# Kernel tuning notes

Hardware: AMD Instinct MI355X
Metric: run time of the kernel (lower is better)

## Reference

```python
import jax, jax.numpy as jnp
import numpy as np

DIM = 512
NH, NKV, HD = 8, 4, DIM // 8
KVD = NKV * HD
EPS = 1.1920928955078125e-07  # torch.finfo(float32).eps (F.rms_norm default)
ROPE_BASE = 10000.0


def _rms_norm(x):
    # F.rms_norm over last dim, no learned weight
    ms = jnp.mean(jnp.square(x), axis=-1, keepdims=True)
    return x * jax.lax.rsqrt(ms + EPS)


def _rope_tables(T, dtype):
    inv_freq = 1.0 / (ROPE_BASE ** (jnp.arange(0, HD, 2, dtype=jnp.float32) / HD))
    t = jnp.arange(T, dtype=jnp.float32)
    f = jnp.outer(t, inv_freq)  # [T, HD//2]
    return jnp.cos(f).astype(dtype)[None, None], jnp.sin(f).astype(dtype)[None, None]


def _apply_rot(x, c, s):
    h = x.shape[-1] // 2
    x1, x2 = x[..., :h], x[..., h:]
    return jnp.concatenate((x1 * c + x2 * s, -x1 * s + x2 * c), axis=-1)


def setup_inputs() -> dict:
    key = jax.random.key(0)
    ks = jax.random.split(key, 5)
    B, T = 8, 2048
    x = jax.random.normal(ks[0], (B, T, DIM), dtype=jnp.float32)
    # torch Linear weights: [out_features, in_features]
    Wq = jax.random.normal(ks[1], (DIM, DIM), dtype=jnp.float32) * (DIM ** -0.5)
    Wk = jax.random.normal(ks[2], (KVD, DIM), dtype=jnp.float32) * (DIM ** -0.5)
    Wv = jax.random.normal(ks[3], (KVD, DIM), dtype=jnp.float32) * (DIM ** -0.5)
    Wp = jax.random.normal(ks[4], (DIM, DIM), dtype=jnp.float32) * (DIM ** -0.5)
    return {"x": x, "Wq": Wq, "Wk": Wk, "Wv": Wv, "Wp": Wp}


def reference(x, Wq, Wk, Wv, Wp):
    B, T, C = x.shape
    q = (x @ Wq.T).reshape(B, T, NH, HD).transpose(0, 2, 1, 3)    # [B,NH,T,HD]
    k = (x @ Wk.T).reshape(B, T, NKV, HD).transpose(0, 2, 1, 3)   # [B,NKV,T,HD]
    v = (x @ Wv.T).reshape(B, T, NKV, HD).transpose(0, 2, 1, 3)
    q, k = _rms_norm(q), _rms_norm(k)
    c, s = _rope_tables(T, q.dtype)
    q, k = _apply_rot(q, c, s), _apply_rot(k, c, s)
    rep = NH // NKV
    k = jnp.repeat(k, rep, axis=1)  # GQA expand -> [B,NH,T,HD]
    v = jnp.repeat(v, rep, axis=1)
    scale = 1.0 / jnp.sqrt(jnp.asarray(HD, dtype=q.dtype))
    scores = jnp.einsum('bhqd,bhkd->bhqk', q, k) * scale
    causal = jnp.tril(jnp.ones((T, T), dtype=bool))
    scores = jnp.where(causal[None, None], scores, jnp.finfo(scores.dtype).min)
    attn = jax.nn.softmax(scores, axis=-1)
    y = jnp.einsum('bhqk,bhkd->bhqd', attn, v)
    y = y.transpose(0, 2, 1, 3).reshape(B, T, C)
    return y @ Wp.T
```

## Files before the change

### kernel.cpp

```cpp
#include <hip/hip_runtime.h>
#include <hip/hip_bf16.h>
#include <stdint.h>

typedef __bf16 bf16;
typedef __bf16 bf16x8 __attribute__((ext_vector_type(8)));
typedef __bf16 bf16x4 __attribute__((ext_vector_type(4)));
typedef float f32x4 __attribute__((ext_vector_type(4)));

#define T_SEQ 2048
#define DIM_ 512
#define NH_ 8
#define NKV_ 4
#define HD_ 64
#define BT_ (8 * T_SEQ)
#define NEG_INF (-1e30f)
#define EPS_ 1.1920928955078125e-07f
#define QSCALE 0.18033688011112042f
#define SMAX 12.0f

#define OFF_XB   (size_t)(0)
#define OFF_WQKV (size_t)(16777216)
#define OFF_WP   (size_t)(17825792)
#define OFF_COS  (size_t)(18350080)
#define OFF_SIN  (size_t)(18612224)
#define OFF_QT   (size_t)(18874368)
#define OFF_KT   (size_t)(35651584)
#define OFF_VT   (size_t)(44040192)
#define OFF_Y    (size_t)(52428800)
#define WS_NEEDED (size_t)(69206016)

__device__ inline void mfma16(f32x4& acc, bf16x8 a, bf16x8 b) {
    acc = __builtin_amdgcn_mfma_f32_16x16x32_bf16(a, b, acc, 0, 0, 0);
}

typedef const __attribute__((address_space(1))) uint8_t* gas_ptr;
typedef __attribute__((address_space(3))) uint8_t* las_ptr;
__device__ inline void gload16(const bf16* g, bf16* l) {
    __builtin_amdgcn_global_load_lds((gas_ptr)(const void*)g, (las_ptr)(void*)l, 16, 0, 0);
}

__global__ void prep_kernel(const float* __restrict__ x, const float* __restrict__ wq,
                            const float* __restrict__ wk, const float* __restrict__ wv,
                            const float* __restrict__ wp,
                            bf16* __restrict__ xb, bf16* __restrict__ wqkv,
                            bf16* __restrict__ wpb, float* __restrict__ cosT,
                            float* __restrict__ sinT) {
    int tid = blockIdx.x * blockDim.x + threadIdx.x;
    int stride = gridDim.x * blockDim.x;
    for (int i = tid; i < BT_ * DIM_; i += stride) xb[i] = (bf16)x[i];
    for (int i = tid; i < 1024 * 512; i += stride) {
        int j = i >> 9, k = i & 511;
        float v;
        if (j < 512) v = wq[i];
        else if (j < 768) v = wk[(j - 512) * 512 + k];
        else v = wv[(j - 768) * 512 + k];
        wqkv[i] = (bf16)v;
    }
    for (int i = tid; i < 512 * 512; i += stride) wpb[i] = (bf16)wp[i];
    for (int i = tid; i < T_SEQ * 32; i += stride) {
        int t = i >> 5, d = i & 31;
        float inv = powf(10000.0f, -(float)d * (1.0f / 32.0f));
        float f = (float)t * inv;
        cosT[i] = cosf(f);
        sinT[i] = sinf(f);
    }
}

__global__ __launch_bounds__(256) void qkv_gemm(const bf16* __restrict__ A,
                                                const bf16* __restrict__ B,
                                                bf16* __restrict__ qt,
                                                bf16* __restrict__ kt,
                                                bf16* __restrict__ vt,
                                                const float* __restrict__ cosT,
                                                const float* __restrict__ sinT) {
    __shared__ __align__(16) char smem[34816];
    bf16* As = (bf16*)smem;
    bf16* Bs = (bf16*)(smem + 16384);
    const int tid = threadIdx.x, lane = tid & 63, wid = tid >> 6;
    const int wr = wid >> 1, wc = wid & 1;
    const int lm = lane & 15, hi = lane >> 4;
    const int bid = blockIdx.x;
    const int swz = (bid & 7) * 128 + (bid >> 3);
    const int brow = (swz & 127) * 128;
    const int bcol = (swz >> 7) * 128;

    f32x4 acc[4][4] = {};
    for (int k0 = 0; k0 < 512; k0 += 64) {
        __syncthreads();
#pragma unroll
        for (int i = 0; i < 4; ++i) {
            int c = i * 256 + tid;
            int slot = c >> 6, l = c & 63;
            int row = (slot >> 1) * 16 + (l & 15);
            int kc = (slot & 1) * 32 + (l >> 4) * 8;
            gload16(A + (size_t)(brow + row) * 512 + k0 + kc, As + c * 8);
            gload16(B + (size_t)(bcol + row) * 512 + k0 + kc, Bs + c * 8);
        }
        asm volatile("s_waitcnt vmcnt(0)" ::: "memory");
        __syncthreads();
#pragma unroll
        for (int kk = 0; kk < 2; ++kk) {
            bf16x8 af[4], bfr[4];
#pragma unroll
            for (int m = 0; m < 4; ++m)
                af[m] = *(const bf16x8*)(As + (((wr * 4 + m) * 2 + kk) * 64 + lane) * 8);
#pragma unroll
            for (int n = 0; n < 4; ++n)
                bfr[n] = *(const bf16x8*)(Bs + (((wc * 4 + n) * 2 + kk) * 64 + lane) * 8);
            __builtin_amdgcn_s_setprio(1);
#pragma unroll
            for (int m = 0; m < 4; ++m)
#pragma unroll
                for (int n = 0; n < 4; ++n) mfma16(acc[m][n], af[m], bfr[n]);
            __builtin_amdgcn_s_setprio(0);
        }
    }
    __syncthreads();

    bf16* Tb = (bf16*)smem + wid * 4224;
    const int wcol = bcol + wc * 64;
    const int ctype = (wcol < 512) ? 0 : (wcol < 768 ? 1 : 2);

    if (ctype < 2) {
#pragma unroll
        for (int m = 0; m < 4; ++m)
#pragma unroll
            for (int r = 0; r < 4; ++r) {
                float v0 = acc[m][0][r], v1 = acc[m][1][r];
                float v2 = acc[m][2][r], v3 = acc[m][3][r];
                float ss = v0 * v0 + v1 * v1 + v2 * v2 + v3 * v3;
                ss += __shfl_xor(ss, 1);
                ss += __shfl_xor(ss, 2);
                ss += __shfl_xor(ss, 4);
                ss += __shfl_xor(ss, 8);
                float rinv = rsqrtf(ss * (1.0f / 64.0f) + EPS_);
                v0 *= rinv; v1 *= rinv; v2 *= rinv; v3 *= rinv;
                int rl = m * 16 + hi * 4 + r;
                int t = (brow + wr * 64 + rl) & (T_SEQ - 1);
                float c0 = cosT[t * 32 + lm], s0 = sinT[t * 32 + lm];
                float c1 = cosT[t * 32 + 16 + lm], s1 = sinT[t * 32 + 16 + lm];
                float o0 = v0 * c0 + v2 * s0;
                float o2 = v2 * c0 - v0 * s0;
                float o1 = v1 * c1 + v3 * s1;
                float o3 = v3 * c1 - v1 * s1;
                if (ctype == 0) { o0 *= QSCALE; o1 *= QSCALE; o2 *= QSCALE; o3 *= QSCALE; }
                Tb[rl * 66 + lm]      = (bf16)o0;
                Tb[rl * 66 + 16 + lm] = (bf16)o1;
                Tb[rl * 66 + 32 + lm] = (bf16)o2;
                Tb[rl * 66 + 48 + lm] = (bf16)o3;
            }
    } else {
#pragma unroll
        for (int m = 0; m < 4; ++m)
#pragma unroll
            for (int n = 0; n < 4; ++n)
#pragma unroll
                for (int r = 0; r < 4; ++r)
                    Tb[(n * 16 + lm) * 66 + m * 16 + hi * 4 + r] = (bf16)acc[m][n][r];
    }
    __syncthreads();

    const int i0 = brow + wr * 64;
    const int b = i0 >> 11, tt = i0 & (T_SEQ - 1);
#pragma unroll
    for (int p = 0; p < 8; ++p) {
        int row = p * 8 + (lane >> 3);
        int ch = lane & 7;
        bf16x8 val = *(const bf16x8*)(Tb + row * 66 + ch * 8);
        if (ctype == 0) {
            int head = wcol >> 6;
            *(bf16x8*)(qt + ((size_t)((b << 3) + head) * T_SEQ + tt + row) * 64 + ch * 8) = val;
        } else if (ctype == 1) {
            int head = (wcol - 512) >> 6;
            *(bf16x8*)(kt + ((size_t)((b << 2) + head) * T_SEQ + tt + row) * 64 + ch * 8) = val;
        } else {
            int head = (wcol - 768) >> 6;
            *(bf16x8*)(vt + ((size_t)((b << 2) + head) * 64 + row) * T_SEQ + tt + ch * 8) = val;
        }
    }
}

__global__ __launch_bounds__(256, 4) void attn_kernel(const bf16* __restrict__ qt,
                                                      const bf16* __restrict__ kt,
                                                      const bf16* __restrict__ vt,
                                                      bf16* __restrict__ y) {
    __shared__ bf16 Klds[4096];
    __shared__ bf16 Vlds[4096];
    __shared__ bf16 Plds[4][32 * 40];
    const int tid = threadIdx.x;
    const int lane = tid & 63, wid = tid >> 6;
    const int lm = lane & 15, hi = lane >> 4;
    const int bh = blockIdx.x & 63;
    const int p = 15 - (int)(blockIdx.x >> 6);
    const int b = bh >> 3, h = bh & 7, hv = h >> 1;
    const bf16* Q = qt + (size_t)bh * T_SEQ * HD_;
    const bf16* K = kt + (size_t)(b * NKV_ + hv) * T_SEQ * HD_;
    const bf16* V = vt + (size_t)(b * NKV_ + hv) * HD_ * T_SEQ;
    const int qB = p * 128;
    const int qw = qB + wid * 32;
    bf16* Pl = &Plds[wid][0];

    const int sl0 = tid >> 6, l0 = tid & 63;
    const int gr0 = (sl0 >> 1) * 16 + (l0 & 15);
    const int gc0 = (sl0 & 1) * 32 + (l0 >> 4) * 8;
    const int sl1 = (256 + tid) >> 6;
    const int gr1 = (sl1 >> 1) * 16 + (l0 & 15);
    const int gc1 = (sl1 & 1) * 32 + (l0 >> 4) * 8;
    const bf16* kg0 = K + (size_t)gr0 * HD_ + gc0;
    const bf16* kg1 = K + (size_t)gr1 * HD_ + gc1;
    const bf16* vg0 = V + (size_t)gr0 * T_SEQ + gc0;
    const bf16* vg1 = V + (size_t)gr1 * T_SEQ + gc1;
    bf16* kd0 = Klds + (size_t)tid * 8;
    bf16* kd1 = Klds + (size_t)(256 + tid) * 8;
    bf16* vd0 = Vlds + (size_t)tid * 8;
    bf16* vd1 = Vlds + (size_t)(256 + tid) * 8;

    bf16x8 qf[2][2];
#pragma unroll
    for (int qm = 0; qm < 2; ++qm)
#pragma unroll
        for (int kk = 0; kk < 2; ++kk)
            qf[qm][kk] = *(const bf16x8*)(Q + (size_t)(qw + 16 * qm + lm) * HD_ + 32 * kk + 8 * hi);

    f32x4 o[2][4] = {};
    float lrow[2] = {0.f, 0.f};

    const int nt = (qB >> 6) + 2;
    for (int t = 0; t < nt; ++t) {
        const int kv0 = t << 6;
        __syncthreads();
        {
            size_t ko = (size_t)kv0 * HD_, vo = (size_t)kv0;
            gload16(kg0 + ko, kd0);
            gload16(kg1 + ko, kd1);
            gload16(vg0 + vo, vd0);
            gload16(vg1 + vo, vd1);
        }
        asm volatile("s_waitcnt vmcnt(0)" ::: "memory");
        __syncthreads();

        if (kv0 <= qw + 31) {
            f32x4 s[2][4] = {};
#pragma unroll
            for (int kk = 0; kk < 2; ++kk) {
                bf16x8 kf[4];
#pragma unroll
                for (int n = 0; n < 4; ++n)
                    kf[n] = *(const bf16x8*)(Klds + ((n * 2 + kk) * 64 + lane) * 8);
#pragma unroll
                for (int qm = 0; qm < 2; ++qm)
#pragma unroll
                    for (int n = 0; n < 4; ++n) mfma16(s[qm][n], kf[n], qf[qm][kk]);
            }
            const bool partial = (kv0 + 63 > qw);
            bf16x4 pw[2][4];
#pragma unroll
            for (int qm = 0; qm < 2; ++qm) {
                const int qg = qw + 16 * qm + lm;
                float ps = 0.f;
#pragma unroll
                for (int n = 0; n < 4; ++n)
#pragma unroll
                    for (int r = 0; r < 4; ++r) {
                        float xv = s[qm][n][r];
                        if (partial)
                            xv = ((kv0 + 16 * n + 4 * hi + r) <= qg) ? xv : NEG_INF;
                        float e = __builtin_amdgcn_exp2f(xv - SMAX);
                        ps += e;
                        pw[qm][n][r] = (bf16)e;
                    }
                ps += __shfl_xor(ps, 16);
                ps += __shfl_xor(ps, 32);
                lrow[qm] += ps;
            }
#pragma unroll
            for (int kk = 0; kk < 2; ++kk) {
#pragma unroll
                for (int qm = 0; qm < 2; ++qm) {
                    *(bf16x4*)(Pl + (16 * qm + lm) * 40 + 4 * hi)      = pw[qm][2 * kk];
                    *(bf16x4*)(Pl + (16 * qm + lm) * 40 + 16 + 4 * hi) = pw[qm][2 * kk + 1];
                }
                bf16x8 vf[4], pf[2];
#pragma unroll
                for (int qm = 0; qm < 2; ++qm)
                    pf[qm] = *(const bf16x8*)(Pl + (16 * qm + lm) * 40 + 8 * hi);
#pragma unroll
                for (int nd = 0; nd < 4; ++nd)
                    vf[nd] = *(const bf16x8*)(Vlds + ((nd * 2 + kk) * 64 + lane) * 8);
#pragma unroll
                for (int qm = 0; qm < 2; ++qm)
#pragma unroll
                    for (int nd = 0; nd < 4; ++nd) mfma16(o[qm][nd], vf[nd], pf[qm]);
            }
        }
    }

#pragma unroll
    for (int qm = 0; qm < 2; ++qm) {
        float rcl = 1.0f / lrow[qm];
#pragma unroll
        for (int nd = 0; nd < 4; ++nd) {
            bf16x4 ov;
#pragma unroll
            for (int r = 0; r < 4; ++r) ov[r] = (bf16)(o[qm][nd][r] * rcl);
            *(bf16x4*)(Pl + lm * 72 + nd * 16 + 4 * hi) = ov;
        }
#pragma unroll
        for (int it = 0; it < 2; ++it) {
            int chunk = it * 64 + lane;
            int row = chunk >> 3, dc = (chunk & 7) * 8;
            bf16x8 val = *(const bf16x8*)(Pl + row * 72 + dc);
            *(bf16x8*)(y + (size_t)(b * T_SEQ + qw + 16 * qm + row) * DIM_ + h * HD_ + dc) = val;
        }
    }
}

__global__ __launch_bounds__(256) void proj_gemm(const bf16* __restrict__ A,
                                                 const bf16* __restrict__ B,
                                                 float* __restrict__ out) {
    __shared__ __align__(16) char smem[32768];
    bf16* As = (bf16*)smem;
    bf16* Bs = (bf16*)(smem + 16384);
    const int tid = threadIdx.x, lane = tid & 63, wid = tid >> 6;
    const int wr = wid >> 1, wc = wid & 1;
    const int lm = lane & 15, hi = lane >> 4;
    const int bid = blockIdx.x;
    const int swz = (bid & 7) * 64 + (bid >> 3);
    const int brow = (swz & 127) * 128;
    const int bcol = (swz >> 7) * 128;

    f32x4 acc[4][4] = {};
    for (int k0 = 0; k0 < 512; k0 += 64) {
        __syncthreads();
#pragma unroll
        for (int i = 0; i < 4; ++i) {
            int c = i * 256 + tid;
            int slot = c >> 6, l = c & 63;
            int row = (slot >> 1) * 16 + (l & 15);
            int kc = (slot & 1) * 32 + (l >> 4) * 8;
            gload16(A + (size_t)(brow + row) * 512 + k0 + kc, As + c * 8);
            gload16(B + (size_t)(bcol + row) * 512 + k0 + kc, Bs + c * 8);
        }
        asm volatile("s_waitcnt vmcnt(0)" ::: "memory");
        __syncthreads();
#pragma unroll
        for (int kk = 0; kk < 2; ++kk) {
            bf16x8 af[4], bfr[4];
#pragma unroll
            for (int m = 0; m < 4; ++m)
                af[m] = *(const bf16x8*)(As + (((wr * 4 + m) * 2 + kk) * 64 + lane) * 8);
#pragma unroll
            for (int n = 0; n < 4; ++n)
                bfr[n] = *(const bf16x8*)(Bs + (((wc * 4 + n) * 2 + kk) * 64 + lane) * 8);
            __builtin_amdgcn_s_setprio(1);
#pragma unroll
            for (int m = 0; m < 4; ++m)
#pragma unroll
                for (int n = 0; n < 4; ++n) mfma16(acc[m][n], af[m], bfr[n]);
            __builtin_amdgcn_s_setprio(0);
        }
    }
#pragma unroll
    for (int m = 0; m < 4; ++m)
#pragma unroll
        for (int n = 0; n < 4; ++n)
#pragma unroll
            for (int r = 0; r < 4; ++r) {
                int i = brow + wr * 64 + m * 16 + hi * 4 + r;
                int j = bcol + wc * 64 + n * 16 + lm;
                out[(size_t)i * DIM_ + j] = acc[m][n][r];
            }
}

extern "C" void kernel_launch(void* const* d_in, const int* in_sizes, int n_in,
                              void* d_out, int out_size, void* d_ws, size_t ws_size,
                              hipStream_t stream) {
    const float* x  = (const float*)d_in[0];
    const float* wq = (const float*)d_in[1];
    const float* wk = (const float*)d_in[2];
    const float* wv = (const float*)d_in[3];
    const float* wp = (const float*)d_in[4];
    if (ws_size < WS_NEEDED) return;

    char* ws = (char*)d_ws;
    bf16* xb    = (bf16*)(ws + OFF_XB);
    bf16* wqkv  = (bf16*)(ws + OFF_WQKV);
    bf16* wpb   = (bf16*)(ws + OFF_WP);
    float* cosT = (float*)(ws + OFF_COS);
    float* sinT = (float*)(ws + OFF_SIN);
    bf16* qt    = (bf16*)(ws + OFF_QT);
    bf16* kt    = (bf16*)(ws + OFF_KT);
    bf16* vt    = (bf16*)(ws + OFF_VT);
    bf16* y     = (bf16*)(ws + OFF_Y);

    prep_kernel<<<2048, 256, 0, stream>>>(x, wq, wk, wv, wp, xb, wqkv, wpb, cosT, sinT);

    qkv_gemm<<<1024, 256, 0, stream>>>(xb, wqkv, qt, kt, vt, cosT, sinT);

    attn_kernel<<<dim3(16 * 64), 256, 0, stream>>>(qt, kt, vt, y);

    proj_gemm<<<512, 256, 0, stream>>>(y, wpb, (float*)d_out);
}
```

Measured before the change: 154.7 us.

## Register-prefetch next K/V tile and reorder causal block schedule

The attention loop now loads the next K/V tile from global memory into registers while computing on the current one, then stores those registers to LDS after a barrier. This replaces the synchronous load-then-wait pattern, so global latency is hidden behind the MFMA work. The block-to-query-tile mapping is also permuted so that heavy and light causal tiles are interleaved across dispatch waves, to balance load. The cost is extra registers for prefetch buffers and raw s_barrier calls whose waitcnt handling must stay correct.

```diff
diff --git a/kernel.cpp b/kernel.cpp
--- a/kernel.cpp
+++ b/kernel.cpp
@@ -190,8 +190,11 @@
     const int tid = threadIdx.x;
     const int lane = tid & 63, wid = tid >> 6;
     const int lm = lane & 15, hi = lane >> 4;
-    const int bh = blockIdx.x & 63;
-    const int p = 15 - (int)(blockIdx.x >> 6);
+    const int bid = blockIdx.x;
+    const int s4 = bid >> 8;
+    const int g4 = (bid >> 6) & 3;
+    const int bh = bid & 63;
+    const int p = 4 * (3 - s4) + ((g4 + s4) & 3);
     const int b = bh >> 3, h = bh & 7, hv = h >> 1;
     const bf16* Q = qt + (size_t)bh * T_SEQ * HD_;
     const bf16* K = kt + (size_t)(b * NKV_ + hv) * T_SEQ * HD_;
@@ -226,18 +229,24 @@
     float lrow[2] = {0.f, 0.f};
 
     const int nt = (qB >> 6) + 2;
+    int4 rk0 = *(const int4*)kg0, rk1 = *(const int4*)kg1;
+    int4 rv0 = *(const int4*)vg0, rv1 = *(const int4*)vg1;
+
     for (int t = 0; t < nt; ++t) {
         const int kv0 = t << 6;
-        __syncthreads();
-        {
-            size_t ko = (size_t)kv0 * HD_, vo = (size_t)kv0;
-            gload16(kg0 + ko, kd0);
-            gload16(kg1 + ko, kd1);
-            gload16(vg0 + vo, vd0);
-            gload16(vg1 + vo, vd1);
-        }
-        asm volatile("s_waitcnt vmcnt(0)" ::: "memory");
-        __syncthreads();
+        __builtin_amdgcn_s_barrier();
+        __builtin_amdgcn_sched_barrier(0);
+        *(int4*)kd0 = rk0; *(int4*)kd1 = rk1;
+        *(int4*)vd0 = rv0; *(int4*)vd1 = rv1;
+        if (t + 1 < nt) {
+            size_t ko = (size_t)(kv0 + 64) * HD_;
+            size_t vo = (size_t)(kv0 + 64);
+            rk0 = *(const int4*)(kg0 + ko); rk1 = *(const int4*)(kg1 + ko);
+            rv0 = *(const int4*)(vg0 + vo); rv1 = *(const int4*)(vg1 + vo);
+        }
+        asm volatile("s_waitcnt lgkmcnt(0)" ::: "memory");
+        __builtin_amdgcn_s_barrier();
+        __builtin_amdgcn_sched_barrier(0);
 
         if (kv0 <= qw + 31) {
             f32x4 s[2][4] = {};
@@ -295,6 +304,7 @@
         }
     }
 
+    __builtin_amdgcn_s_barrier();
 #pragma unroll
     for (int qm = 0; qm < 2; ++qm) {
         float rcl = 1.0f / lrow[qm];
```

Result: slower. 170.4 us (+10.1%).
